# Performance work log

Measured on AMD Instinct MI355X. Metric: run time of the kernel, lower is better.

Reference implementation:

```python
import jax, jax.numpy as jnp
import numpy as np

DIN = 1024   # input_embedding_size
D = 128      # embedding_size
N, T = 4, 4096


def setup_inputs() -> dict:
    key = jax.random.key(0)
    kx, kq, kk, kv = jax.random.split(key, 4)
    x = jax.random.normal(kx, (N, T, DIN), dtype=jnp.float32)
    # torch Linear(DIN, D, bias=False): weight [D, DIN], y = x @ W.T.
    # Store transposed [DIN, D] so q = x @ Wq is the same math.
    s = 1.0 / np.sqrt(DIN)
    Wq = jax.random.uniform(kq, (DIN, D), jnp.float32, -s, s)
    Wk = jax.random.uniform(kk, (DIN, D), jnp.float32, -s, s)
    Wv = jax.random.uniform(kv, (DIN, D), jnp.float32, -s, s)
    return {"x": x, "Wq": Wq, "Wk": Wk, "Wv": Wv}


def reference(x, Wq, Wk, Wv):
    # x: [N,T,DIN]
    q = jnp.einsum('ntc,cd->ntd', x, Wq)  # [N,T,D]
    k = jnp.einsum('ntc,cd->ntd', x, Wk)
    v = jnp.einsum('ntc,cd->ntd', x, Wv)
    att = jnp.einsum('ntd,nsd->nts', q, k)  # [N,T,T], no 1/sqrt(D) scaling (faithful)
    Tlen = x.shape[1]
    causal = jnp.tril(jnp.ones((Tlen, Tlen), dtype=bool))
    # faithful to torch: tril() zeros upper triangle, then masked_fill(att == 0, -inf)
    att = jnp.where(causal, att, 0.0)
    att = jnp.where(att == 0.0, -jnp.inf, att)
    att = jax.nn.softmax(att, axis=-1)  # [N,T,T]
    out = jnp.einsum('nts,nsd->ntd', att, v)  # [N,T,D]
    return out, att
```

## Files before the change

kernel.cpp:

```cpp
#include <hip/hip_runtime.h>

typedef _Float16 f16;
typedef __attribute__((ext_vector_type(8))) _Float16 f16x8;
typedef __attribute__((ext_vector_type(8))) short s16x8;
typedef __attribute__((ext_vector_type(4))) float f32x4;

#define DIN   1024
#define DD    128
#define NBAT  4
#define TLEN  4096

static __device__ __forceinline__ unsigned short f2bf(float f) {
  unsigned int u = __builtin_bit_cast(unsigned int, f);
  u = (u + 0x7fffu + ((u >> 16) & 1u)) >> 16;
  return (unsigned short)u;
}
static __device__ __forceinline__ float bf2f(unsigned short h) {
  return __builtin_bit_cast(float, (unsigned int)h << 16);
}
static __device__ __forceinline__ unsigned short f2h(float f) {
  _Float16 h = (_Float16)f;
  return __builtin_bit_cast(unsigned short, h);
}
static __device__ __forceinline__ int swz128(int d, int key) {
  return ((((d >> 3) ^ key) & 15) << 3) | (d & 7);
}

typedef __attribute__((address_space(1))) const unsigned int* gas1_t;
typedef __attribute__((address_space(3))) unsigned int* las3_t;
static __device__ __forceinline__ void gload16(const void* g, void* l) {
  __builtin_amdgcn_global_load_lds((gas1_t)g, (las3_t)l, 16, 0, 0);
}

__global__ void xcast(const float* __restrict__ x,
                      unsigned short* __restrict__ xh, unsigned short* __restrict__ xl) {
  size_t i = ((size_t)blockIdx.x * 256 + threadIdx.x) * 8;
  f32x4 a0 = *(const f32x4*)(x + i);
  f32x4 a1 = *(const f32x4*)(x + i + 4);
  s16x8 hv, lv;
#pragma unroll
  for (int e = 0; e < 4; ++e) {
    unsigned short h0 = f2bf(a0[e]);
    hv[e] = (short)h0; lv[e] = (short)f2bf(a0[e] - bf2f(h0));
    unsigned short h1 = f2bf(a1[e]);
    hv[4 + e] = (short)h1; lv[4 + e] = (short)f2bf(a1[e] - bf2f(h1));
  }
  *(s16x8*)(xh + i) = hv;
  *(s16x8*)(xl + i) = lv;
}

__global__ void build_wt(const float* __restrict__ Wq, const float* __restrict__ Wk,
                         const float* __restrict__ Wv,
                         unsigned short* __restrict__ Wh, unsigned short* __restrict__ Wl) {
  int col = blockIdx.x;
  const float* W = (col < 128) ? Wq : (col < 256 ? Wk : Wv);
  int j = col & 127;
  for (int kk = (int)threadIdx.x; kk < DIN; kk += blockDim.x) {
    float w = W[(size_t)kk * DD + j];
    unsigned short h = f2bf(w);
    unsigned short l = f2bf(w - bf2f(h));
    Wh[(size_t)col * DIN + kk] = h;
    Wl[(size_t)col * DIN + kk] = l;
  }
}

__global__ __launch_bounds__(256, 2) void proj_qkv(
    const unsigned short* __restrict__ xh, const unsigned short* __restrict__ xl,
    const unsigned short* __restrict__ Wh, const unsigned short* __restrict__ Wl,
    unsigned short* __restrict__ qws, unsigned short* __restrict__ kws,
    unsigned short* __restrict__ vws) {
  __shared__ __align__(16) unsigned short vt[128 * 40];

  const int tid = (int)threadIdx.x;
  const int lane = tid & 63;
  const int wid = tid >> 6;
  const int lr = lane & 15;
  const int lg = lane >> 4;
  const int t0 = blockIdx.x * 32;

  f32x4 acc[2][6];
#pragma unroll
  for (int a = 0; a < 2; ++a)
#pragma unroll
    for (int b = 0; b < 6; ++b) acc[a][b] = f32x4{0.f, 0.f, 0.f, 0.f};

  for (int kc = 0; kc < 32; ++kc) {
    s16x8 ah[2], al[2];
#pragma unroll
    for (int rf = 0; rf < 2; ++rf) {
      size_t aoff = (size_t)(t0 + rf * 16 + lr) * DIN + kc * 32 + lg * 8;
      ah[rf] = *(const s16x8*)(xh + aoff);
      al[rf] = *(const s16x8*)(xl + aoff);
    }
#pragma unroll
    for (int cf = 0; cf < 6; ++cf) {
      size_t boff = (size_t)(wid * 96 + cf * 16 + lr) * DIN + kc * 32 + lg * 8;
      s16x8 bh = *(const s16x8*)(Wh + boff);
      s16x8 bl = *(const s16x8*)(Wl + boff);
#pragma unroll
      for (int rf = 0; rf < 2; ++rf) {
        acc[rf][cf] = __builtin_amdgcn_mfma_f32_16x16x32_bf16(ah[rf], bh, acc[rf][cf], 0, 0, 0);
        acc[rf][cf] = __builtin_amdgcn_mfma_f32_16x16x32_bf16(ah[rf], bl, acc[rf][cf], 0, 0, 0);
        acc[rf][cf] = __builtin_amdgcn_mfma_f32_16x16x32_bf16(al[rf], bh, acc[rf][cf], 0, 0, 0);
      }
    }
  }

  const int n = t0 >> 12, t0l = t0 & (TLEN - 1);
#pragma unroll
  for (int cf = 0; cf < 6; ++cf) {
    int c = wid * 96 + cf * 16 + lr;
#pragma unroll
    for (int rf = 0; rf < 2; ++rf)
#pragma unroll
      for (int e = 0; e < 4; ++e) {
        int tl = rf * 16 + lg * 4 + e;
        int t = t0 + tl;
        unsigned short hv = f2h(acc[rf][cf][e]);
        if (c < 128) {
          qws[(size_t)t * DD + c] = hv;
        } else if (c < 256) {
          kws[(size_t)t * DD + swz128(c - 128, t & 7)] = hv;
        } else {
          vt[(c - 256) * 40 + tl] = hv;
        }
      }
  }
  __syncthreads();
  if (tid < 128) {
    int d = tid;
    int ch = t0l >> 7, pos0 = t0l & 127;
    unsigned short* dst = vws + ((size_t)n * DD + d) * TLEN + ch * 128;
#pragma unroll
    for (int h = 0; h < 4; ++h) {
      f16x8 vv = *(const f16x8*)&vt[d * 40 + h * 8];
      int g = (((pos0 + h * 8) >> 3) ^ (d & 7)) << 3;
      *(f16x8*)(dst + g) = vv;
    }
  }
}

__global__ __launch_bounds__(512, 4) void attn_fused(
    const unsigned short* __restrict__ qws, const unsigned short* __restrict__ kws,
    const unsigned short* __restrict__ vws, float* __restrict__ out,
    float* __restrict__ att) {
  __shared__ __align__(16) unsigned short kvbuf[32768];
  __shared__ __align__(16) unsigned short pp[8][16 * 40];
  __shared__ float zb[8][16];
  __shared__ float rzb[32];
  unsigned short* kl = kvbuf;
  unsigned short* vl = kvbuf + 16384;

  const int tid = (int)threadIdx.x;
  const int lane = tid & 63;
  const int wid = tid >> 6;
  const int lr = lane & 15;
  const int lg = lane >> 4;
  const int rg = wid >> 2;
  const int cg = wid & 3;

  int b = (int)blockIdx.x;
  int cr = (b < 256) ? b : (767 - b);
  const int qi = cr >> 2;
  const int n = cr & 3;
  const int t0 = qi * 32;
  const int jmax = (t0 + 31) >> 7;

  const unsigned short* kbase = kws + (size_t)(n * TLEN) * DD;
  const unsigned short* vbase = vws + (size_t)n * DD * TLEN;
  float* attn_base = att + (size_t)n * TLEN * TLEN + (size_t)t0 * TLEN;

  {
    int cz0 = (jmax + 1) * 128;
    f32x4 zv = f32x4{0.f, 0.f, 0.f, 0.f};
    for (int r = 0; r < 32; ++r) {
      float* rowp = attn_base + (size_t)r * TLEN;
      for (int c = cz0 + tid * 4; c < TLEN; c += 2048) *(f32x4*)(rowp + c) = zv;
    }
  }

  f16x8 qa[4];
  {
    const unsigned short* q0 = qws + (size_t)(n * TLEN + t0 + rg * 16 + lr) * DD + lg * 8;
#pragma unroll
    for (int kc = 0; kc < 4; ++kc) qa[kc] = *(const f16x8*)(q0 + kc * 32);
  }
  const int rowl0 = rg * 16 + lg * 4;

  float zacc[4] = {0.f, 0.f, 0.f, 0.f};
  for (int j = 0; j <= jmax; ++j) {
    const char* gk = (const char*)(kbase + (size_t)(j * 128) * DD);
#pragma unroll
    for (int rr = 0; rr < 4; ++rr) {
      int idx = rr * 512 + tid;
      gload16(gk + (size_t)idx * 16, (char*)kl + (size_t)idx * 16);
    }
    __syncthreads();
#pragma unroll
    for (int cf = 0; cf < 2; ++cf) {
      int krow = cg * 32 + cf * 16 + lr;
      f32x4 s = f32x4{0.f, 0.f, 0.f, 0.f};
#pragma unroll
      for (int kc = 0; kc < 4; ++kc) {
        f16x8 kb = *(const f16x8*)&kl[krow * 128 + ((((kc * 4 + lg) ^ (krow & 7))) << 3)];
        s = __builtin_amdgcn_mfma_f32_16x16x32_f16(qa[kc], kb, s, 0, 0, 0);
      }
      int colg = j * 128 + krow;
#pragma unroll
      for (int e = 0; e < 4; ++e) {
        int rowg = t0 + rowl0 + e;
        zacc[e] += (colg <= rowg && s[e] != 0.0f) ? __expf(s[e]) : 0.0f;
      }
    }
    __syncthreads();
  }
#pragma unroll
  for (int e = 0; e < 4; ++e) {
    float z = zacc[e];
    z += __shfl_xor(z, 1);
    z += __shfl_xor(z, 2);
    z += __shfl_xor(z, 4);
    z += __shfl_xor(z, 8);
    if (lr == 0) zb[wid][lg * 4 + e] = z;
  }
  __syncthreads();
  if (tid < 32) {
    int r = tid, rgq = r >> 4, rl = r & 15;
    float z = zb[rgq * 4 + 0][rl] + zb[rgq * 4 + 1][rl] + zb[rgq * 4 + 2][rl] + zb[rgq * 4 + 3][rl];
    rzb[r] = (z > 0.f) ? (1.0f / z) : 0.0f;
  }
  __syncthreads();
  float rz[4];
#pragma unroll
  for (int e = 0; e < 4; ++e) rz[e] = rzb[rowl0 + e];

  f32x4 oacc[8];
#pragma unroll
  for (int fd = 0; fd < 8; ++fd) oacc[fd] = f32x4{0.f, 0.f, 0.f, 0.f};
  unsigned short* ppw = pp[wid];

  for (int j = 0; j <= jmax; ++j) {
    const char* gk = (const char*)(kbase + (size_t)(j * 128) * DD);
#pragma unroll
    for (int rr = 0; rr < 4; ++rr) {
      int idx = rr * 512 + tid;
      gload16(gk + (size_t)idx * 16, (char*)kl + (size_t)idx * 16);
    }
#pragma unroll
    for (int rr = 0; rr < 4; ++rr) {
      int idx = rr * 512 + tid;
      int d = idx >> 4, off = idx & 15;
      gload16((const char*)(vbase + ((size_t)d * TLEN + j * 128 + off * 8)),
              (char*)vl + (size_t)idx * 16);
    }
    __syncthreads();

#pragma unroll
    for (int cf = 0; cf < 2; ++cf) {
      int krow = cg * 32 + cf * 16 + lr;
      f32x4 s = f32x4{0.f, 0.f, 0.f, 0.f};
#pragma unroll
      for (int kc = 0; kc < 4; ++kc) {
        f16x8 kb = *(const f16x8*)&kl[krow * 128 + ((((kc * 4 + lg) ^ (krow & 7))) << 3)];
        s = __builtin_amdgcn_mfma_f32_16x16x32_f16(qa[kc], kb, s, 0, 0, 0);
      }
      int colg = j * 128 + krow;
#pragma unroll
      for (int e = 0; e < 4; ++e) {
        int rowg = t0 + rowl0 + e;
        float ev = (colg <= rowg && s[e] != 0.0f) ? __expf(s[e]) : 0.0f;
        float p = ev * rz[e];
        attn_base[(size_t)(rowl0 + e) * TLEN + colg] = p;
        ppw[(lg * 4 + e) * 40 + cf * 16 + lr] = f2h(p);
      }
    }
    f16x8 pa = *(const f16x8*)&ppw[lr * 40 + lg * 8];
#pragma unroll
    for (int fd = 0; fd < 8; ++fd) {
      int d = fd * 16 + lr;
      f16x8 vb = *(const f16x8*)&vl[d * 128 + ((((cg * 4 + lg) ^ (d & 7))) << 3)];
      oacc[fd] = __builtin_amdgcn_mfma_f32_16x16x32_f16(pa, vb, oacc[fd], 0, 0, 0);
    }
    __syncthreads();
  }

  float* red = (float*)kvbuf;
#pragma unroll
  for (int fd = 0; fd < 8; ++fd)
#pragma unroll
    for (int e = 0; e < 4; ++e)
      red[((size_t)wid * 16 + lg * 4 + e) * 128 + fd * 16 + lr] = oacc[fd][e];
  __syncthreads();
  {
    int r = tid >> 4;
    int d0 = (tid & 15) * 8;
    int rgq = r >> 4, rl = r & 15;
    f32x4 s0 = f32x4{0.f, 0.f, 0.f, 0.f}, s1 = f32x4{0.f, 0.f, 0.f, 0.f};
#pragma unroll
    for (int c = 0; c < 4; ++c) {
      const float* src = red + ((size_t)(rgq * 4 + c) * 16 + rl) * 128 + d0;
      f32x4 a = *(const f32x4*)src;
      f32x4 bb = *(const f32x4*)(src + 4);
#pragma unroll
      for (int i = 0; i < 4; ++i) { s0[i] += a[i]; s1[i] += bb[i]; }
    }
    float* dst = out + ((size_t)n * TLEN + t0 + r) * DD + d0;
    *(f32x4*)dst = s0;
    *(f32x4*)(dst + 4) = s1;
  }
}

extern "C" void kernel_launch(void* const* d_in, const int* in_sizes, int n_in,
                              void* d_out, int out_size, void* d_ws, size_t ws_size,
                              hipStream_t stream) {
  const float* x  = (const float*)d_in[0];
  const float* Wq = (const float*)d_in[1];
  const float* Wk = (const float*)d_in[2];
  const float* Wv = (const float*)d_in[3];

  float* out = (float*)d_out;
  float* att = out + (size_t)NBAT * TLEN * DD;

  unsigned short* ws = (unsigned short*)d_ws;
  unsigned short* Wh  = ws;
  unsigned short* Wl  = Wh + (size_t)384 * DIN;
  unsigned short* xh  = Wl + (size_t)384 * DIN;
  unsigned short* xl  = xh + (size_t)NBAT * TLEN * DIN;
  unsigned short* qws = xl + (size_t)NBAT * TLEN * DIN;
  unsigned short* kws = qws + (size_t)NBAT * TLEN * DD;
  unsigned short* vws = kws + (size_t)NBAT * TLEN * DD;

  xcast<<<dim3(8192), dim3(256), 0, stream>>>(x, xh, xl);
  build_wt<<<dim3(384), dim3(256), 0, stream>>>(Wq, Wk, Wv, Wh, Wl);
  proj_qkv<<<dim3(512), dim3(256), 0, stream>>>(xh, xl, Wh, Wl, qws, kws, vws);
  attn_fused<<<dim3(512), dim3(512), 0, stream>>>(qws, kws, vws, out, att);
}
```

Before: 532.4 us.

## Fuse x bf16 split into projection, double-buffer K tiles, read V from global

```diff
diff --git a/kernel.cpp b/kernel.cpp
--- a/kernel.cpp
+++ b/kernel.cpp
@@ -4,6 +4,7 @@
 typedef __attribute__((ext_vector_type(8))) _Float16 f16x8;
 typedef __attribute__((ext_vector_type(8))) short s16x8;
 typedef __attribute__((ext_vector_type(4))) float f32x4;
+typedef __attribute__((ext_vector_type(4))) unsigned short us16x4;
 
 #define DIN   1024
 #define DD    128
@@ -30,23 +31,6 @@
 typedef __attribute__((address_space(3))) unsigned int* las3_t;
 static __device__ __forceinline__ void gload16(const void* g, void* l) {
   __builtin_amdgcn_global_load_lds((gas1_t)g, (las3_t)l, 16, 0, 0);
-}
-
-__global__ void xcast(const float* __restrict__ x,
-                      unsigned short* __restrict__ xh, unsigned short* __restrict__ xl) {
-  size_t i = ((size_t)blockIdx.x * 256 + threadIdx.x) * 8;
-  f32x4 a0 = *(const f32x4*)(x + i);
-  f32x4 a1 = *(const f32x4*)(x + i + 4);
-  s16x8 hv, lv;
-#pragma unroll
-  for (int e = 0; e < 4; ++e) {
-    unsigned short h0 = f2bf(a0[e]);
-    hv[e] = (short)h0; lv[e] = (short)f2bf(a0[e] - bf2f(h0));
-    unsigned short h1 = f2bf(a1[e]);
-    hv[4 + e] = (short)h1; lv[4 + e] = (short)f2bf(a1[e] - bf2f(h1));
-  }
-  *(s16x8*)(xh + i) = hv;
-  *(s16x8*)(xl + i) = lv;
 }
 
 __global__ void build_wt(const float* __restrict__ Wq, const float* __restrict__ Wk,
@@ -65,10 +49,12 @@
 }
 
 __global__ __launch_bounds__(256, 2) void proj_qkv(
-    const unsigned short* __restrict__ xh, const unsigned short* __restrict__ xl,
+    const float* __restrict__ x,
     const unsigned short* __restrict__ Wh, const unsigned short* __restrict__ Wl,
     unsigned short* __restrict__ qws, unsigned short* __restrict__ kws,
     unsigned short* __restrict__ vws) {
+  __shared__ __align__(16) unsigned short Ah[32 * 64];
+  __shared__ __align__(16) unsigned short Al[32 * 64];
   __shared__ __align__(16) unsigned short vt[128 * 40];
 
   const int tid = (int)threadIdx.x;
@@ -78,32 +64,57 @@
   const int lg = lane >> 4;
   const int t0 = blockIdx.x * 32;
 
+  const int srow = tid >> 3;
+  const int sg = tid & 7;
+  const float* xsrc = x + (size_t)(t0 + srow) * DIN + sg * 8;
+  const int sgs = (sg ^ (srow & 7)) * 8;
+
   f32x4 acc[2][6];
 #pragma unroll
   for (int a = 0; a < 2; ++a)
 #pragma unroll
-    for (int b = 0; b < 6; ++b) acc[a][b] = f32x4{0.f, 0.f, 0.f, 0.f};
-
-  for (int kc = 0; kc < 32; ++kc) {
-    s16x8 ah[2], al[2];
-#pragma unroll
-    for (int rf = 0; rf < 2; ++rf) {
-      size_t aoff = (size_t)(t0 + rf * 16 + lr) * DIN + kc * 32 + lg * 8;
-      ah[rf] = *(const s16x8*)(xh + aoff);
-      al[rf] = *(const s16x8*)(xl + aoff);
-    }
-#pragma unroll
-    for (int cf = 0; cf < 6; ++cf) {
-      size_t boff = (size_t)(wid * 96 + cf * 16 + lr) * DIN + kc * 32 + lg * 8;
-      s16x8 bh = *(const s16x8*)(Wh + boff);
-      s16x8 bl = *(const s16x8*)(Wl + boff);
+    for (int c = 0; c < 6; ++c) acc[a][c] = f32x4{0.f, 0.f, 0.f, 0.f};
+
+  for (int kr = 0; kr < 16; ++kr) {
+    {
+      f32x4 a0 = *(const f32x4*)(xsrc + kr * 64);
+      f32x4 a1 = *(const f32x4*)(xsrc + kr * 64 + 4);
+      s16x8 hv, lv;
+#pragma unroll
+      for (int e = 0; e < 4; ++e) {
+        unsigned short h0 = f2bf(a0[e]);
+        hv[e] = (short)h0; lv[e] = (short)f2bf(a0[e] - bf2f(h0));
+        unsigned short h1 = f2bf(a1[e]);
+        hv[4 + e] = (short)h1; lv[4 + e] = (short)f2bf(a1[e] - bf2f(h1));
+      }
+      *(s16x8*)&Ah[srow * 64 + sgs] = hv;
+      *(s16x8*)&Al[srow * 64 + sgs] = lv;
+    }
+    __syncthreads();
+
+#pragma unroll
+    for (int kc = 0; kc < 2; ++kc) {
+      s16x8 ah[2], al[2];
 #pragma unroll
       for (int rf = 0; rf < 2; ++rf) {
-        acc[rf][cf] = __builtin_amdgcn_mfma_f32_16x16x32_bf16(ah[rf], bh, acc[rf][cf], 0, 0, 0);
-        acc[rf][cf] = __builtin_amdgcn_mfma_f32_16x16x32_bf16(ah[rf], bl, acc[rf][cf], 0, 0, 0);
-        acc[rf][cf] = __builtin_amdgcn_mfma_f32_16x16x32_bf16(al[rf], bh, acc[rf][cf], 0, 0, 0);
-      }
-    }
+        int g = (((kc * 4 + lg) ^ (lr & 7)) << 3);
+        ah[rf] = *(const s16x8*)&Ah[(rf * 16 + lr) * 64 + g];
+        al[rf] = *(const s16x8*)&Al[(rf * 16 + lr) * 64 + g];
+      }
+#pragma unroll
+      for (int cf = 0; cf < 6; ++cf) {
+        size_t boff = (size_t)(wid * 96 + cf * 16 + lr) * DIN + (size_t)kr * 64 + kc * 32 + lg * 8;
+        s16x8 bh = *(const s16x8*)(Wh + boff);
+        s16x8 bl = *(const s16x8*)(Wl + boff);
+#pragma unroll
+        for (int rf = 0; rf < 2; ++rf) {
+          acc[rf][cf] = __builtin_amdgcn_mfma_f32_16x16x32_bf16(ah[rf], bh, acc[rf][cf], 0, 0, 0);
+          acc[rf][cf] = __builtin_amdgcn_mfma_f32_16x16x32_bf16(ah[rf], bl, acc[rf][cf], 0, 0, 0);
+          acc[rf][cf] = __builtin_amdgcn_mfma_f32_16x16x32_bf16(al[rf], bh, acc[rf][cf], 0, 0, 0);
+        }
+      }
+    }
+    __syncthreads();
   }
 
   const int n = t0 >> 12, t0l = t0 & (TLEN - 1);
@@ -129,13 +140,11 @@
   __syncthreads();
   if (tid < 128) {
     int d = tid;
-    int ch = t0l >> 7, pos0 = t0l & 127;
-    unsigned short* dst = vws + ((size_t)n * DD + d) * TLEN + ch * 128;
+    unsigned short* dst = vws + ((size_t)n * DD + d) * TLEN + t0l;
 #pragma unroll
     for (int h = 0; h < 4; ++h) {
       f16x8 vv = *(const f16x8*)&vt[d * 40 + h * 8];
-      int g = (((pos0 + h * 8) >> 3) ^ (d & 7)) << 3;
-      *(f16x8*)(dst + g) = vv;
+      *(f16x8*)(dst + h * 8) = vv;
     }
   }
 }
@@ -144,12 +153,10 @@
     const unsigned short* __restrict__ qws, const unsigned short* __restrict__ kws,
     const unsigned short* __restrict__ vws, float* __restrict__ out,
     float* __restrict__ att) {
-  __shared__ __align__(16) unsigned short kvbuf[32768];
+  __shared__ __align__(16) unsigned short kl[2][16384];
   __shared__ __align__(16) unsigned short pp[8][16 * 40];
   __shared__ float zb[8][16];
   __shared__ float rzb[32];
-  unsigned short* kl = kvbuf;
-  unsigned short* vl = kvbuf + 16384;
 
   const int tid = (int)threadIdx.x;
   const int lane = tid & 63;
@@ -170,6 +177,12 @@
   const unsigned short* vbase = vws + (size_t)n * DD * TLEN;
   float* attn_base = att + (size_t)n * TLEN * TLEN + (size_t)t0 * TLEN;
 
+#pragma unroll
+  for (int rr = 0; rr < 4; ++rr) {
+    int idx = rr * 512 + tid;
+    gload16((const char*)kbase + (size_t)idx * 16, (char*)kl[0] + (size_t)idx * 16);
+  }
+
   {
     int cz0 = (jmax + 1) * 128;
     f32x4 zv = f32x4{0.f, 0.f, 0.f, 0.f};
@@ -189,20 +202,23 @@
 
   float zacc[4] = {0.f, 0.f, 0.f, 0.f};
   for (int j = 0; j <= jmax; ++j) {
-    const char* gk = (const char*)(kbase + (size_t)(j * 128) * DD);
-#pragma unroll
-    for (int rr = 0; rr < 4; ++rr) {
-      int idx = rr * 512 + tid;
-      gload16(gk + (size_t)idx * 16, (char*)kl + (size_t)idx * 16);
-    }
     __syncthreads();
+    if (j < jmax) {
+      const char* gk = (const char*)(kbase + (size_t)((j + 1) * 128) * DD);
+#pragma unroll
+      for (int rr = 0; rr < 4; ++rr) {
+        int idx = rr * 512 + tid;
+        gload16(gk + (size_t)idx * 16, (char*)kl[(j + 1) & 1] + (size_t)idx * 16);
+      }
+    }
+    const unsigned short* klc = kl[j & 1];
 #pragma unroll
     for (int cf = 0; cf < 2; ++cf) {
       int krow = cg * 32 + cf * 16 + lr;
       f32x4 s = f32x4{0.f, 0.f, 0.f, 0.f};
 #pragma unroll
       for (int kc = 0; kc < 4; ++kc) {
-        f16x8 kb = *(const f16x8*)&kl[krow * 128 + ((((kc * 4 + lg) ^ (krow & 7))) << 3)];
+        f16x8 kb = *(const f16x8*)&klc[krow * 128 + ((((kc * 4 + lg) ^ (krow & 7))) << 3)];
         s = __builtin_amdgcn_mfma_f32_16x16x32_f16(qa[kc], kb, s, 0, 0, 0);
       }
       int colg = j * 128 + krow;
@@ -212,7 +228,6 @@
         zacc[e] += (colg <= rowg && s[e] != 0.0f) ? __expf(s[e]) : 0.0f;
       }
     }
-    __syncthreads();
   }
 #pragma unroll
   for (int e = 0; e < 4; ++e) {
@@ -234,41 +249,55 @@
 #pragma unroll
   for (int e = 0; e < 4; ++e) rz[e] = rzb[rowl0 + e];
 
+#pragma unroll
+  for (int rr = 0; rr < 4; ++rr) {
+    int idx = rr * 512 + tid;
+    gload16((const char*)kbase + (size_t)idx * 16, (char*)kl[0] + (size_t)idx * 16);
+  }
+
   f32x4 oacc[8];
 #pragma unroll
   for (int fd = 0; fd < 8; ++fd) oacc[fd] = f32x4{0.f, 0.f, 0.f, 0.f};
   unsigned short* ppw = pp[wid];
 
   for (int j = 0; j <= jmax; ++j) {
-    const char* gk = (const char*)(kbase + (size_t)(j * 128) * DD);
-#pragma unroll
-    for (int rr = 0; rr < 4; ++rr) {
-      int idx = rr * 512 + tid;
-      gload16(gk + (size_t)idx * 16, (char*)kl + (size_t)idx * 16);
-    }
-#pragma unroll
-    for (int rr = 0; rr < 4; ++rr) {
-      int idx = rr * 512 + tid;
-      int d = idx >> 4, off = idx & 15;
-      gload16((const char*)(vbase + ((size_t)d * TLEN + j * 128 + off * 8)),
-              (char*)vl + (size_t)idx * 16);
-    }
     __syncthreads();
-
+    if (j < jmax) {
+      const char* gk = (const char*)(kbase + (size_t)((j + 1) * 128) * DD);
+#pragma unroll
+      for (int rr = 0; rr < 4; ++rr) {
+        int idx = rr * 512 + tid;
+        gload16(gk + (size_t)idx * 16, (char*)kl[(j + 1) & 1] + (size_t)idx * 16);
+      }
+    }
+    const unsigned short* klc = kl[j & 1];
+
+    f32x4 s[2];
 #pragma unroll
     for (int cf = 0; cf < 2; ++cf) {
       int krow = cg * 32 + cf * 16 + lr;
-      f32x4 s = f32x4{0.f, 0.f, 0.f, 0.f};
+      s[cf] = f32x4{0.f, 0.f, 0.f, 0.f};
 #pragma unroll
       for (int kc = 0; kc < 4; ++kc) {
-        f16x8 kb = *(const f16x8*)&kl[krow * 128 + ((((kc * 4 + lg) ^ (krow & 7))) << 3)];
-        s = __builtin_amdgcn_mfma_f32_16x16x32_f16(qa[kc], kb, s, 0, 0, 0);
-      }
+        f16x8 kb = *(const f16x8*)&klc[krow * 128 + ((((kc * 4 + lg) ^ (krow & 7))) << 3)];
+        s[cf] = __builtin_amdgcn_mfma_f32_16x16x32_f16(qa[kc], kb, s[cf], 0, 0, 0);
+      }
+    }
+
+    f16x8 vb[8];
+#pragma unroll
+    for (int fd = 0; fd < 8; ++fd) {
+      vb[fd] = *(const f16x8*)(vbase + (size_t)(fd * 16 + lr) * TLEN + (size_t)j * 128 + cg * 32 + lg * 8);
+    }
+
+#pragma unroll
+    for (int cf = 0; cf < 2; ++cf) {
+      int krow = cg * 32 + cf * 16 + lr;
       int colg = j * 128 + krow;
 #pragma unroll
       for (int e = 0; e < 4; ++e) {
         int rowg = t0 + rowl0 + e;
-        float ev = (colg <= rowg && s[e] != 0.0f) ? __expf(s[e]) : 0.0f;
+        float ev = (colg <= rowg && s[cf][e] != 0.0f) ? __expf(s[cf][e]) : 0.0f;
         float p = ev * rz[e];
         attn_base[(size_t)(rowl0 + e) * TLEN + colg] = p;
         ppw[(lg * 4 + e) * 40 + cf * 16 + lr] = f2h(p);
@@ -277,14 +306,12 @@
     f16x8 pa = *(const f16x8*)&ppw[lr * 40 + lg * 8];
 #pragma unroll
     for (int fd = 0; fd < 8; ++fd) {
-      int d = fd * 16 + lr;
-      f16x8 vb = *(const f16x8*)&vl[d * 128 + ((((cg * 4 + lg) ^ (d & 7))) << 3)];
-      oacc[fd] = __builtin_amdgcn_mfma_f32_16x16x32_f16(pa, vb, oacc[fd], 0, 0, 0);
-    }
-    __syncthreads();
-  }
-
-  float* red = (float*)kvbuf;
+      oacc[fd] = __builtin_amdgcn_mfma_f32_16x16x32_f16(pa, vb[fd], oacc[fd], 0, 0, 0);
+    }
+  }
+
+  __syncthreads();
+  float* red = (float*)kl;
 #pragma unroll
   for (int fd = 0; fd < 8; ++fd)
 #pragma unroll
@@ -324,14 +351,11 @@
   unsigned short* ws = (unsigned short*)d_ws;
   unsigned short* Wh  = ws;
   unsigned short* Wl  = Wh + (size_t)384 * DIN;
-  unsigned short* xh  = Wl + (size_t)384 * DIN;
-  unsigned short* xl  = xh + (size_t)NBAT * TLEN * DIN;
-  unsigned short* qws = xl + (size_t)NBAT * TLEN * DIN;
+  unsigned short* qws = Wl + (size_t)384 * DIN;
   unsigned short* kws = qws + (size_t)NBAT * TLEN * DD;
   unsigned short* vws = kws + (size_t)NBAT * TLEN * DD;
 
-  xcast<<<dim3(8192), dim3(256), 0, stream>>>(x, xh, xl);
   build_wt<<<dim3(384), dim3(256), 0, stream>>>(Wq, Wk, Wv, Wh, Wl);
-  proj_qkv<<<dim3(512), dim3(256), 0, stream>>>(xh, xl, Wh, Wl, qws, kws, vws);
+  proj_qkv<<<dim3(512), dim3(256), 0, stream>>>(x, Wh, Wl, qws, kws, vws);
   attn_fused<<<dim3(512), dim3(512), 0, stream>>>(qws, kws, vws, out, att);
 }
```

After: 534.5 us. No clear change (+0.4%).
